# Kernel optimization log

Hardware: AMD Instinct MI355X
Metric: run time of the kernel (lower is better)

## Reference

```python
import jax, jax.numpy as jnp
import numpy as np

NUM_EXPERTS = 8
TOP_K = 2


def setup_inputs() -> dict:
    key = jax.random.key(0)
    ks = jax.random.split(key, 6)
    B, S, D, H, E = 4, 1024, 1024, 2048, NUM_EXPERTS
    x = jax.random.normal(ks[0], (B, S, D), dtype=jnp.float32)
    Wg = jax.random.normal(ks[1], (D, E), dtype=jnp.float32) * 0.02
    W1 = jax.random.normal(ks[2], (E, D, H), dtype=jnp.float32) * 0.02
    b1 = jax.random.normal(ks[3], (E, H), dtype=jnp.float32) * 0.02
    W2 = jax.random.normal(ks[4], (E, H, D), dtype=jnp.float32) * 0.02
    b2 = jax.random.normal(ks[5], (E, D), dtype=jnp.float32) * 0.02
    return {"x": x, "Wg": Wg, "W1": W1, "b1": b1, "W2": W2, "b2": b2}


def reference(x, Wg, W1, b1, W2, b2):
    B, S, D = x.shape
    E, _, H = W1.shape
    OUT = W2.shape[2]
    xm = x.reshape(-1, D)                      # [N, D], N = B*S
    # --- top-k gating (ProbabilitySamplerTopk): softmax over experts, take top-k ---
    logits = xm @ Wg                           # [N, E]
    probs = jax.nn.softmax(logits, axis=-1)
    topk_p, topk_i = jax.lax.top_k(probs, TOP_K)   # [N, K]
    # --- sort dispatched (token, expert) pairs by expert id (stable) ---
    flat_e = topk_i.reshape(-1)                # [N*K]
    flat_p = topk_p.reshape(-1)                # [N*K]
    order = jnp.argsort(flat_e)                # stable sort -> grouped by expert
    tok_idx = order // TOP_K                   # source token index (trunc-div by topK)
    e_sorted = flat_e[order]                   # [N*K]
    p_sorted = flat_p[order]                   # [N*K]
    xs = xm[tok_idx]                           # [N*K, D] expert-sorted inputs
    # --- grouped-GEMM experts: masked per-expert dense GEMM (E is small & fixed) ---
    y = jnp.zeros((xs.shape[0], OUT), dtype=xs.dtype)
    for e in range(E):
        h = jax.nn.relu(xs @ W1[e] + b1[e])    # [N*K, H]
        ye = h @ W2[e] + b2[e]                 # [N*K, OUT]
        m = (e_sorted == e)[:, None].astype(xs.dtype)
        y = y + m * ye
    # --- combine: multiply by gates, scatter-add back to token slots ---
    y = y * p_sorted[:, None]
    out = jnp.zeros((B * S, OUT), dtype=y.dtype).at[tok_idx].add(y)
    return out.reshape(B, S, OUT)
```

## Files before the change

### kernel.cpp

```cpp
#include <hip/hip_runtime.h>
#include <hip/hip_bf16.h>
#include <stdint.h>

typedef __bf16 bf16;
typedef __bf16 bf16x8 __attribute__((ext_vector_type(8)));
typedef __bf16 bf16x4 __attribute__((ext_vector_type(4)));
typedef float f32x4 __attribute__((ext_vector_type(4)));

#define N_TOK 4096
#define DDIM 1024
#define HDIM 2048
#define NPAIR 8192

__device__ __forceinline__ void gload16(const void* g, void* l) {
  __builtin_amdgcn_global_load_lds(
      (const __attribute__((address_space(1))) unsigned int*)g,
      (__attribute__((address_space(3))) unsigned int*)l, 16, 0, 0);
}

__global__ void transpose_cvt_kernel(const float* __restrict__ in, bf16* __restrict__ out,
                                     int R, int C) {
  __shared__ float tile[32][33];
  const float* ip = in + (size_t)blockIdx.z * R * C;
  bf16* op = out + (size_t)blockIdx.z * R * C;
  int r0 = blockIdx.y * 32, c0 = blockIdx.x * 32;
  int tr = threadIdx.x >> 3;
  int tc = (threadIdx.x & 7) * 4;
  float4 v = *(const float4*)(ip + (size_t)(r0 + tr) * C + c0 + tc);
  tile[tr][tc] = v.x; tile[tr][tc + 1] = v.y; tile[tr][tc + 2] = v.z; tile[tr][tc + 3] = v.w;
  __syncthreads();
  bf16x4 o = {(bf16)tile[tc + 0][tr], (bf16)tile[tc + 1][tr],
              (bf16)tile[tc + 2][tr], (bf16)tile[tc + 3][tr]};
  *(bf16x4*)(op + (size_t)(c0 + tr) * R + r0 + tc) = o;
}

__global__ void gate_kernel(const float* __restrict__ x, const float* __restrict__ Wg,
                            int2* __restrict__ ge, float2* __restrict__ gp,
                            bf16* __restrict__ xb, float* __restrict__ outp) {
  int t0 = blockIdx.x * 4;
  {
    float4 z = make_float4(0.f, 0.f, 0.f, 0.f);
    float4* ob = (float4*)(outp + (size_t)t0 * DDIM);
#pragma unroll
    for (int r = 0; r < 4; r++) ob[r * 256 + threadIdx.x] = z;
  }
  int t = t0 + (threadIdx.x >> 6);
  int lane = threadIdx.x & 63;
  const float* xr = x + (size_t)t * DDIM;
  bf16* xbr = xb + (size_t)t * DDIM;
  float a[8];
#pragma unroll
  for (int e = 0; e < 8; e++) a[e] = 0.f;
#pragma unroll
  for (int it = 0; it < 4; it++) {
    int d0 = it * 256 + lane * 4;
    float4 xv = *(const float4*)(xr + d0);
    bf16x4 o = {(bf16)xv.x, (bf16)xv.y, (bf16)xv.z, (bf16)xv.w};
    *(bf16x4*)(xbr + d0) = o;
    float xs[4] = {xv.x, xv.y, xv.z, xv.w};
#pragma unroll
    for (int dd = 0; dd < 4; dd++) {
      float4 w0 = *(const float4*)(Wg + (size_t)(d0 + dd) * 8);
      float4 w1 = *(const float4*)(Wg + (size_t)(d0 + dd) * 8 + 4);
      a[0] += xs[dd] * w0.x; a[1] += xs[dd] * w0.y; a[2] += xs[dd] * w0.z; a[3] += xs[dd] * w0.w;
      a[4] += xs[dd] * w1.x; a[5] += xs[dd] * w1.y; a[6] += xs[dd] * w1.z; a[7] += xs[dd] * w1.w;
    }
  }
#pragma unroll
  for (int off = 32; off >= 1; off >>= 1) {
#pragma unroll
    for (int e = 0; e < 8; e++) a[e] += __shfl_xor(a[e], off);
  }
  if (lane == 0) {
    float m = a[0];
#pragma unroll
    for (int e = 1; e < 8; e++) m = fmaxf(m, a[e]);
    float p[8]; float s = 0.f;
#pragma unroll
    for (int e = 0; e < 8; e++) { p[e] = expf(a[e] - m); s += p[e]; }
    float inv = 1.f / s;
    int i0 = 0; float v0 = a[0];
#pragma unroll
    for (int e = 1; e < 8; e++) if (a[e] > v0) { v0 = a[e]; i0 = e; }
    int i1 = -1; float v1 = -1e30f;
#pragma unroll
    for (int e = 0; e < 8; e++) if (e != i0 && a[e] > v1) { v1 = a[e]; i1 = e; }
    ge[t] = make_int2(i0, i1);
    gp[t] = make_float2(p[i0] * inv, p[i1] * inv);
  }
}

__global__ void sort_kernel(const int2* __restrict__ ge, const float2* __restrict__ gp,
                            int* __restrict__ tok, float* __restrict__ ps,
                            int* __restrict__ meta) {
  __shared__ int hist[8], runn[8], wc[16][8], wb[16][8], baseS[9];
  int tid = threadIdx.x;
  int lane = tid & 63, wv = tid >> 6;
  if (tid < 8) hist[tid] = 0;
  __syncthreads();
  for (int i = tid; i < NPAIR; i += 1024) {
    int2 g = ge[i >> 1];
    int e = (i & 1) ? g.y : g.x;
    atomicAdd(&hist[e], 1);
  }
  __syncthreads();
  if (tid == 0) {
    int b = 0, ts1 = 0;
    for (int e = 0; e < 8; e++) {
      baseS[e] = b; meta[e] = b;
      meta[9 + e] = ts1;  ts1 += (hist[e] + 127) / 128;
      b += hist[e];
    }
    baseS[8] = b; meta[8] = b; meta[17] = ts1;
  }
  __syncthreads();
  if (tid < 8) runn[tid] = baseS[tid];
  __syncthreads();
  for (int c = 0; c < 8; c++) {
    int i = c * 1024 + tid;
    int2 g = ge[i >> 1];
    int e = (i & 1) ? g.y : g.x;
    int rank = 0;
#pragma unroll
    for (int ee = 0; ee < 8; ee++) {
      unsigned long long b = __ballot(e == ee);
      if (e == ee) rank = __popcll(b & ((1ull << lane) - 1ull));
      if (lane == 0) wc[wv][ee] = __popcll(b);
    }
    __syncthreads();
    if (tid < 8) {
      int s = runn[tid];
      for (int w = 0; w < 16; w++) { wb[w][tid] = s; s += wc[w][tid]; }
      runn[tid] = s;
    }
    __syncthreads();
    int pos = wb[wv][e] + rank;
    tok[pos] = i >> 1;
    float2 p2 = gp[i >> 1];
    ps[pos] = (i & 1) ? p2.y : p2.x;
    __syncthreads();
  }
}

template <int KDIM, int NPE, bool FIRST, int NT>
__global__ __launch_bounds__(256, 2)
void moe_gemm_kernel(const bf16* __restrict__ A, const bf16* __restrict__ Bt,
                     const float* __restrict__ bias, const int* __restrict__ tok,
                     const float* __restrict__ ps, const int* __restrict__ meta,
                     bf16* __restrict__ hout, float* __restrict__ outp) {
  __shared__ bf16 lds[3][12288];
  constexpr int nk = KDIM / 32;

  int MTa = meta[17];
  int xcd = blockIdx.x & 7;
  int idx = blockIdx.x >> 3;
  int mLo = (MTa * xcd) >> 3;
  int mHi = (MTa * (xcd + 1)) >> 3;
  int cnt = mHi - mLo;
  if (idx >= cnt * NT) return;
  int tileN = idx / cnt;
  int tileM = mLo + idx - tileN * cnt;

  int e = 0;
#pragma unroll
  for (int k = 1; k < 8; k++) if (tileM >= meta[9 + k]) e = k;
  int row0 = meta[e] + (tileM - meta[9 + e]) * 128;
  int segEnd = meta[e + 1];
  int n0 = tileN * 256;

  int t = threadIdx.x;
  int swz = ((t & 3) ^ ((t >> 3) & 3)) * 8;
  const bf16* aSrc[2];
  const bf16* bSrc[4];
#pragma unroll
  for (int u = 0; u < 2; u++) {
    int row = u * 64 + (t >> 2);
    int gRow = row0 + row; if (gRow > NPAIR - 1) gRow = NPAIR - 1;
    int arow = FIRST ? tok[gRow] : gRow;
    aSrc[u] = A + (size_t)arow * KDIM + swz;
  }
#pragma unroll
  for (int u = 0; u < 4; u++) {
    int row = u * 64 + (t >> 2);
    bSrc[u] = Bt + ((size_t)e * NPE + n0 + row) * KDIM + swz;
  }

  int lane = t & 63, wv = t >> 6;
  int wm = wv >> 1, wn = wv & 1;
  int l15 = lane & 15, l4 = lane >> 4;
  int aOff[4], bOff[8];
#pragma unroll
  for (int m = 0; m < 4; m++) {
    int row = wm * 64 + m * 16 + l15;
    aOff[m] = row * 32 + ((l4 ^ ((row >> 1) & 3)) * 8);
  }
#pragma unroll
  for (int n = 0; n < 8; n++) {
    int row = wn * 128 + n * 16 + l15;
    bOff[n] = 4096 + row * 32 + ((l4 ^ ((row >> 1) & 3)) * 8);
  }

  f32x4 acc[4][8];
#pragma unroll
  for (int m = 0; m < 4; m++)
#pragma unroll
    for (int n = 0; n < 8; n++)
#pragma unroll
      for (int j = 0; j < 4; j++) acc[m][n][j] = 0.f;

  auto SA = [&](int j, int u) {
    gload16(aSrc[u] + j * 32, &lds[j % 3][0] + u * 2048 + t * 8);
  };
  auto SB = [&](int j, int u) {
    gload16(bSrc[u] + j * 32, &lds[j % 3][0] + 4096 + u * 2048 + t * 8);
  };

  SA(0, 0); SA(0, 1); SB(0, 0); SB(0, 1); SB(0, 2); SB(0, 3);
  SA(1, 0); SA(1, 1); SB(1, 0); SB(1, 1); SB(1, 2); SB(1, 3);
  asm volatile("s_waitcnt vmcnt(6)\n\ts_barrier" ::: "memory");

  for (int j = 0; j < nk; j++) {
    const bf16* sb = &lds[j % 3][0];
    bf16x8 af[4], bfr[4];
#pragma unroll
    for (int m = 0; m < 4; m++) af[m] = *(const bf16x8*)(sb + aOff[m]);
#pragma unroll
    for (int n = 0; n < 4; n++) bfr[n] = *(const bf16x8*)(sb + bOff[n]);
    if (j + 2 < nk) {
      SA(j + 2, 0); SA(j + 2, 1); SB(j + 2, 0);
      asm volatile("s_waitcnt vmcnt(3)\n\ts_barrier" ::: "memory");
    } else {
      asm volatile("s_waitcnt vmcnt(0)\n\ts_barrier" ::: "memory");
    }
    asm volatile("s_waitcnt lgkmcnt(0)" ::: "memory");
    __builtin_amdgcn_sched_barrier(0);
    __builtin_amdgcn_s_setprio(1);
#pragma unroll
    for (int m = 0; m < 4; m++)
#pragma unroll
      for (int n = 0; n < 4; n++)
        acc[m][n] = __builtin_amdgcn_mfma_f32_16x16x32_bf16(af[m], bfr[n], acc[m][n], 0, 0, 0);
    __builtin_amdgcn_s_setprio(0);
    __builtin_amdgcn_s_barrier();
#pragma unroll
    for (int n = 0; n < 4; n++) bfr[n] = *(const bf16x8*)(sb + bOff[4 + n]);
    if (j + 2 < nk) { SB(j + 2, 1); SB(j + 2, 2); SB(j + 2, 3); }
    __builtin_amdgcn_s_barrier();
    asm volatile("s_waitcnt lgkmcnt(0)" ::: "memory");
    __builtin_amdgcn_sched_barrier(0);
    __builtin_amdgcn_s_setprio(1);
#pragma unroll
    for (int m = 0; m < 4; m++)
#pragma unroll
      for (int n = 0; n < 4; n++)
        acc[m][4 + n] = __builtin_amdgcn_mfma_f32_16x16x32_bf16(af[m], bfr[n], acc[m][4 + n], 0, 0, 0);
    __builtin_amdgcn_s_setprio(0);
    __builtin_amdgcn_s_barrier();
  }

  int colb = n0 + wn * 128 + l15;
  float bia[8];
#pragma unroll
  for (int n = 0; n < 8; n++) bia[n] = bias[(size_t)e * NPE + colb + n * 16];
#pragma unroll
  for (int m = 0; m < 4; m++) {
#pragma unroll
    for (int jj = 0; jj < 4; jj++) {
      int gRow = row0 + wm * 64 + m * 16 + l4 * 4 + jj;
      if (gRow < segEnd) {
        if (FIRST) {
#pragma unroll
          for (int n = 0; n < 8; n++) {
            float v = acc[m][n][jj] + bia[n];
            v = fmaxf(v, 0.f);
            hout[(size_t)gRow * NPE + colb + n * 16] = (bf16)v;
          }
        } else {
          float pscale = ps[gRow];
          float* orow = outp + (size_t)tok[gRow] * DDIM;
#pragma unroll
          for (int n = 0; n < 8; n++) {
            float v = (acc[m][n][jj] + bia[n]) * pscale;
            atomicAdd(orow + colb + n * 16, v);
          }
        }
      }
    }
  }
}

extern "C" void kernel_launch(void* const* d_in, const int* in_sizes, int n_in,
                              void* d_out, int out_size, void* d_ws, size_t ws_size,
                              hipStream_t stream) {
  (void)in_sizes; (void)n_in; (void)out_size; (void)ws_size;
  const float* x  = (const float*)d_in[0];
  const float* Wg = (const float*)d_in[1];
  const float* W1 = (const float*)d_in[2];
  const float* b1 = (const float*)d_in[3];
  const float* W2 = (const float*)d_in[4];
  const float* b2 = (const float*)d_in[5];
  float* out = (float*)d_out;

  char* ws = (char*)d_ws;
  bf16*  xb   = (bf16*)(ws);
  bf16*  W1T  = (bf16*)(ws + (8ull  << 20));
  bf16*  W2T  = (bf16*)(ws + (40ull << 20));
  bf16*  hbuf = (bf16*)(ws + (72ull << 20));
  char*  ext  = ws + (104ull << 20);
  int2*   ge      = (int2*)(ext);
  float2* gp      = (float2*)(ext + (64u  << 10));
  int*    tok     = (int*)(ext + (128u << 10));
  float*  psarr   = (float*)(ext + (160u << 10));
  int*    meta    = (int*)(ext + (224u << 10));

  transpose_cvt_kernel<<<dim3(64, 32, 8), 256, 0, stream>>>(W1, W1T, 1024, 2048);
  transpose_cvt_kernel<<<dim3(32, 64, 8), 256, 0, stream>>>(W2, W2T, 2048, 1024);
  gate_kernel<<<1024, 256, 0, stream>>>(x, Wg, ge, gp, xb, out);
  sort_kernel<<<1, 1024, 0, stream>>>(ge, gp, tok, psarr, meta);
  moe_gemm_kernel<1024, 2048, true, 8><<<dim3(576), 256, 0, stream>>>(
      xb, W1T, b1, tok, psarr, meta, hbuf, nullptr);
  moe_gemm_kernel<2048, 1024, false, 4><<<dim3(288), 256, 0, stream>>>(
      hbuf, W2T, b2, tok, psarr, meta, nullptr, out);
}
```

Measured before the change: 203.1 us.

## Use 256x256 tiles with 512 threads and split-K for second GEMM

Both expert GEMMs move from 128x256 tiles with 256 threads to 256x256 tiles with 512 threads (8 waves), doubling per-block data reuse and reorganising the LDS pipeline. The second GEMM is split along K into two halves written to separate fp32 buffers, which a new combine kernel sums into the output. This is meant to raise arithmetic intensity and balance the grid to a fixed 320 blocks, at the cost of an extra zeroing pass, extra buffer traffic, more tile padding for small expert segments, and lower occupancy.

```diff
diff --git a/kernel.cpp b/kernel.cpp
--- a/kernel.cpp
+++ b/kernel.cpp
@@ -7,7 +7,6 @@
 typedef __bf16 bf16x4 __attribute__((ext_vector_type(4)));
 typedef float f32x4 __attribute__((ext_vector_type(4)));
 
-#define N_TOK 4096
 #define DDIM 1024
 #define HDIM 2048
 #define NPAIR 8192
@@ -36,13 +35,18 @@
 
 __global__ void gate_kernel(const float* __restrict__ x, const float* __restrict__ Wg,
                             int2* __restrict__ ge, float2* __restrict__ gp,
-                            bf16* __restrict__ xb, float* __restrict__ outp) {
+                            bf16* __restrict__ xb, float* __restrict__ y2a,
+                            float* __restrict__ y2b) {
   int t0 = blockIdx.x * 4;
   {
     float4 z = make_float4(0.f, 0.f, 0.f, 0.f);
-    float4* ob = (float4*)(outp + (size_t)t0 * DDIM);
-#pragma unroll
-    for (int r = 0; r < 4; r++) ob[r * 256 + threadIdx.x] = z;
+    float4* za = (float4*)(y2a + (size_t)t0 * DDIM);
+    float4* zb = (float4*)(y2b + (size_t)t0 * DDIM);
+#pragma unroll
+    for (int r = 0; r < 4; r++) {
+      za[r * 256 + threadIdx.x] = z;
+      zb[r * 256 + threadIdx.x] = z;
+    }
   }
   int t = t0 + (threadIdx.x >> 6);
   int lane = threadIdx.x & 63;
@@ -105,13 +109,13 @@
   }
   __syncthreads();
   if (tid == 0) {
-    int b = 0, ts1 = 0;
+    int b = 0, ts = 0;
     for (int e = 0; e < 8; e++) {
       baseS[e] = b; meta[e] = b;
-      meta[9 + e] = ts1;  ts1 += (hist[e] + 127) / 128;
+      meta[9 + e] = ts; ts += (hist[e] + 255) / 256;
       b += hist[e];
     }
-    baseS[8] = b; meta[8] = b; meta[17] = ts1;
+    baseS[8] = b; meta[8] = b; meta[17] = ts;
   }
   __syncthreads();
   if (tid < 8) runn[tid] = baseS[tid];
@@ -142,14 +146,19 @@
   }
 }
 
-template <int KDIM, int NPE, bool FIRST, int NT>
-__global__ __launch_bounds__(256, 2)
+template <bool FIRST>
+__global__ __launch_bounds__(512, 1)
 void moe_gemm_kernel(const bf16* __restrict__ A, const bf16* __restrict__ Bt,
                      const float* __restrict__ bias, const int* __restrict__ tok,
                      const float* __restrict__ ps, const int* __restrict__ meta,
-                     bf16* __restrict__ hout, float* __restrict__ outp) {
-  __shared__ bf16 lds[3][12288];
-  constexpr int nk = KDIM / 32;
+                     bf16* __restrict__ hout, float* __restrict__ y2a,
+                     float* __restrict__ y2b) {
+  constexpr int AK  = FIRST ? DDIM : HDIM;
+  constexpr int BK  = FIRST ? DDIM : HDIM;
+  constexpr int NPE = FIRST ? HDIM : DDIM;
+  constexpr int NT  = 8;
+  constexpr int nk  = 32;
+  __shared__ bf16 lds[3][16384];
 
   int MTa = meta[17];
   int xcd = blockIdx.x & 7;
@@ -164,129 +173,129 @@
   int e = 0;
 #pragma unroll
   for (int k = 1; k < 8; k++) if (tileM >= meta[9 + k]) e = k;
-  int row0 = meta[e] + (tileM - meta[9 + e]) * 128;
+  int row0 = meta[e] + (tileM - meta[9 + e]) * 256;
   int segEnd = meta[e + 1];
-  int n0 = tileN * 256;
+  int n0, kOff;
+  if (FIRST) { n0 = tileN * 256; kOff = 0; }
+  else       { n0 = (tileN & 3) * 256; kOff = (tileN >> 2) * 1024; }
 
   int t = threadIdx.x;
   int swz = ((t & 3) ^ ((t >> 3) & 3)) * 8;
   const bf16* aSrc[2];
-  const bf16* bSrc[4];
+  const bf16* bSrc[2];
 #pragma unroll
   for (int u = 0; u < 2; u++) {
-    int row = u * 64 + (t >> 2);
+    int row = u * 128 + (t >> 2);
     int gRow = row0 + row; if (gRow > NPAIR - 1) gRow = NPAIR - 1;
     int arow = FIRST ? tok[gRow] : gRow;
-    aSrc[u] = A + (size_t)arow * KDIM + swz;
-  }
-#pragma unroll
-  for (int u = 0; u < 4; u++) {
-    int row = u * 64 + (t >> 2);
-    bSrc[u] = Bt + ((size_t)e * NPE + n0 + row) * KDIM + swz;
+    aSrc[u] = A + (size_t)arow * AK + kOff + swz;
+    bSrc[u] = Bt + ((size_t)e * NPE + n0 + row) * BK + kOff + swz;
   }
 
   int lane = t & 63, wv = t >> 6;
-  int wm = wv >> 1, wn = wv & 1;
+  int wm = wv >> 2, wn = wv & 3;
   int l15 = lane & 15, l4 = lane >> 4;
-  int aOff[4], bOff[8];
-#pragma unroll
-  for (int m = 0; m < 4; m++) {
-    int row = wm * 64 + m * 16 + l15;
-    aOff[m] = row * 32 + ((l4 ^ ((row >> 1) & 3)) * 8);
-  }
-#pragma unroll
-  for (int n = 0; n < 8; n++) {
-    int row = wn * 128 + n * 16 + l15;
-    bOff[n] = 4096 + row * 32 + ((l4 ^ ((row >> 1) & 3)) * 8);
-  }
-
-  f32x4 acc[4][8];
-#pragma unroll
-  for (int m = 0; m < 4; m++)
-#pragma unroll
-    for (int n = 0; n < 8; n++)
-#pragma unroll
-      for (int j = 0; j < 4; j++) acc[m][n][j] = 0.f;
+  int aOff[8], bOff[4];
+#pragma unroll
+  for (int mf = 0; mf < 8; mf++) {
+    int row = wm * 128 + mf * 16 + l15;
+    aOff[mf] = row * 32 + ((l4 ^ ((row >> 1) & 3)) * 8);
+  }
+#pragma unroll
+  for (int nf = 0; nf < 4; nf++) {
+    int row = wn * 64 + nf * 16 + l15;
+    bOff[nf] = 8192 + row * 32 + ((l4 ^ ((row >> 1) & 3)) * 8);
+  }
+
+  f32x4 acc[8][4];
+#pragma unroll
+  for (int mf = 0; mf < 8; mf++)
+#pragma unroll
+    for (int nf = 0; nf < 4; nf++)
+#pragma unroll
+      for (int j = 0; j < 4; j++) acc[mf][nf][j] = 0.f;
 
   auto SA = [&](int j, int u) {
-    gload16(aSrc[u] + j * 32, &lds[j % 3][0] + u * 2048 + t * 8);
+    gload16(aSrc[u] + j * 32, &lds[j % 3][0] + u * 4096 + t * 8);
   };
   auto SB = [&](int j, int u) {
-    gload16(bSrc[u] + j * 32, &lds[j % 3][0] + 4096 + u * 2048 + t * 8);
+    gload16(bSrc[u] + j * 32, &lds[j % 3][0] + 8192 + u * 4096 + t * 8);
   };
 
-  SA(0, 0); SA(0, 1); SB(0, 0); SB(0, 1); SB(0, 2); SB(0, 3);
-  SA(1, 0); SA(1, 1); SB(1, 0); SB(1, 1); SB(1, 2); SB(1, 3);
-  asm volatile("s_waitcnt vmcnt(6)\n\ts_barrier" ::: "memory");
+  SA(0, 0); SA(0, 1); SB(0, 0); SB(0, 1);
+  SA(1, 0); SA(1, 1); SB(1, 0); SB(1, 1);
 
   for (int j = 0; j < nk; j++) {
     const bf16* sb = &lds[j % 3][0];
+    if (j + 2 < nk) { SA(j + 2, 0); SA(j + 2, 1); }
+    if (j + 2 < nk)      asm volatile("s_waitcnt vmcnt(6)\n\ts_barrier" ::: "memory");
+    else if (j + 1 < nk) asm volatile("s_waitcnt vmcnt(4)\n\ts_barrier" ::: "memory");
+    else                 asm volatile("s_waitcnt vmcnt(0)\n\ts_barrier" ::: "memory");
     bf16x8 af[4], bfr[4];
 #pragma unroll
-    for (int m = 0; m < 4; m++) af[m] = *(const bf16x8*)(sb + aOff[m]);
-#pragma unroll
-    for (int n = 0; n < 4; n++) bfr[n] = *(const bf16x8*)(sb + bOff[n]);
-    if (j + 2 < nk) {
-      SA(j + 2, 0); SA(j + 2, 1); SB(j + 2, 0);
-      asm volatile("s_waitcnt vmcnt(3)\n\ts_barrier" ::: "memory");
-    } else {
-      asm volatile("s_waitcnt vmcnt(0)\n\ts_barrier" ::: "memory");
-    }
+    for (int mf = 0; mf < 4; mf++) af[mf] = *(const bf16x8*)(sb + aOff[mf]);
+#pragma unroll
+    for (int nf = 0; nf < 4; nf++) bfr[nf] = *(const bf16x8*)(sb + bOff[nf]);
     asm volatile("s_waitcnt lgkmcnt(0)" ::: "memory");
     __builtin_amdgcn_sched_barrier(0);
     __builtin_amdgcn_s_setprio(1);
 #pragma unroll
-    for (int m = 0; m < 4; m++)
-#pragma unroll
-      for (int n = 0; n < 4; n++)
-        acc[m][n] = __builtin_amdgcn_mfma_f32_16x16x32_bf16(af[m], bfr[n], acc[m][n], 0, 0, 0);
+    for (int mf = 0; mf < 4; mf++)
+#pragma unroll
+      for (int nf = 0; nf < 4; nf++)
+        acc[mf][nf] = __builtin_amdgcn_mfma_f32_16x16x32_bf16(af[mf], bfr[nf], acc[mf][nf], 0, 0, 0);
     __builtin_amdgcn_s_setprio(0);
-    __builtin_amdgcn_s_barrier();
-#pragma unroll
-    for (int n = 0; n < 4; n++) bfr[n] = *(const bf16x8*)(sb + bOff[4 + n]);
-    if (j + 2 < nk) { SB(j + 2, 1); SB(j + 2, 2); SB(j + 2, 3); }
-    __builtin_amdgcn_s_barrier();
+    if (j + 2 < nk) { SB(j + 2, 0); SB(j + 2, 1); }
+#pragma unroll
+    for (int mf = 0; mf < 4; mf++) af[mf] = *(const bf16x8*)(sb + aOff[4 + mf]);
     asm volatile("s_waitcnt lgkmcnt(0)" ::: "memory");
     __builtin_amdgcn_sched_barrier(0);
     __builtin_amdgcn_s_setprio(1);
 #pragma unroll
-    for (int m = 0; m < 4; m++)
-#pragma unroll
-      for (int n = 0; n < 4; n++)
-        acc[m][4 + n] = __builtin_amdgcn_mfma_f32_16x16x32_bf16(af[m], bfr[n], acc[m][4 + n], 0, 0, 0);
+    for (int mf = 0; mf < 4; mf++)
+#pragma unroll
+      for (int nf = 0; nf < 4; nf++)
+        acc[4 + mf][nf] = __builtin_amdgcn_mfma_f32_16x16x32_bf16(af[mf], bfr[nf], acc[4 + mf][nf], 0, 0, 0);
     __builtin_amdgcn_s_setprio(0);
     __builtin_amdgcn_s_barrier();
   }
 
-  int colb = n0 + wn * 128 + l15;
-  float bia[8];
-#pragma unroll
-  for (int n = 0; n < 8; n++) bia[n] = bias[(size_t)e * NPE + colb + n * 16];
-#pragma unroll
-  for (int m = 0; m < 4; m++) {
+  int colb = n0 + wn * 64 + l15;
+  float bia[4];
+#pragma unroll
+  for (int nf = 0; nf < 4; nf++)
+    bia[nf] = (FIRST || kOff == 0) ? bias[(size_t)e * NPE + colb + nf * 16] : 0.f;
+  float* ybuf = FIRST ? nullptr : ((kOff == 0) ? y2a : y2b);
+#pragma unroll
+  for (int mf = 0; mf < 8; mf++) {
 #pragma unroll
     for (int jj = 0; jj < 4; jj++) {
-      int gRow = row0 + wm * 64 + m * 16 + l4 * 4 + jj;
+      int gRow = row0 + wm * 128 + mf * 16 + l4 * 4 + jj;
       if (gRow < segEnd) {
         if (FIRST) {
 #pragma unroll
-          for (int n = 0; n < 8; n++) {
-            float v = acc[m][n][jj] + bia[n];
-            v = fmaxf(v, 0.f);
-            hout[(size_t)gRow * NPE + colb + n * 16] = (bf16)v;
+          for (int nf = 0; nf < 4; nf++) {
+            float v = acc[mf][nf][jj] + bia[nf];
+            hout[(size_t)gRow * HDIM + colb + nf * 16] = (bf16)fmaxf(v, 0.f);
           }
         } else {
           float pscale = ps[gRow];
-          float* orow = outp + (size_t)tok[gRow] * DDIM;
-#pragma unroll
-          for (int n = 0; n < 8; n++) {
-            float v = (acc[m][n][jj] + bia[n]) * pscale;
-            atomicAdd(orow + colb + n * 16, v);
-          }
+          float* orow = ybuf + (size_t)tok[gRow] * DDIM;
+#pragma unroll
+          for (int nf = 0; nf < 4; nf++)
+            atomicAdd(orow + colb + nf * 16, (acc[mf][nf][jj] + bia[nf]) * pscale);
         }
       }
     }
   }
+}
+
+__global__ void combine_kernel(const float* __restrict__ a, const float* __restrict__ b,
+                               float* __restrict__ out) {
+  int i = blockIdx.x * 256 + threadIdx.x;
+  f32x4 va = ((const f32x4*)a)[i];
+  f32x4 vb = ((const f32x4*)b)[i];
+  ((f32x4*)out)[i] = va + vb;
 }
 
 extern "C" void kernel_launch(void* const* d_in, const int* in_sizes, int n_in,
@@ -306,7 +315,9 @@
   bf16*  W1T  = (bf16*)(ws + (8ull  << 20));
   bf16*  W2T  = (bf16*)(ws + (40ull << 20));
   bf16*  hbuf = (bf16*)(ws + (72ull << 20));
-  char*  ext  = ws + (104ull << 20);
+  float* y2a  = (float*)(ws + (104ull << 20));
+  float* y2b  = (float*)(ws + (120ull << 20));
+  char*  ext  = ws + (136ull << 20);
   int2*   ge      = (int2*)(ext);
   float2* gp      = (float2*)(ext + (64u  << 10));
   int*    tok     = (int*)(ext + (128u << 10));
@@ -315,10 +326,11 @@
 
   transpose_cvt_kernel<<<dim3(64, 32, 8), 256, 0, stream>>>(W1, W1T, 1024, 2048);
   transpose_cvt_kernel<<<dim3(32, 64, 8), 256, 0, stream>>>(W2, W2T, 2048, 1024);
-  gate_kernel<<<1024, 256, 0, stream>>>(x, Wg, ge, gp, xb, out);
+  gate_kernel<<<1024, 256, 0, stream>>>(x, Wg, ge, gp, xb, y2a, y2b);
   sort_kernel<<<1, 1024, 0, stream>>>(ge, gp, tok, psarr, meta);
-  moe_gemm_kernel<1024, 2048, true, 8><<<dim3(576), 256, 0, stream>>>(
-      xb, W1T, b1, tok, psarr, meta, hbuf, nullptr);
-  moe_gemm_kernel<2048, 1024, false, 4><<<dim3(288), 256, 0, stream>>>(
-      hbuf, W2T, b2, tok, psarr, meta, nullptr, out);
-}
+  moe_gemm_kernel<true><<<dim3(320), 512, 0, stream>>>(
+      xb, W1T, b1, tok, psarr, meta, hbuf, nullptr, nullptr);
+  moe_gemm_kernel<false><<<dim3(320), 512, 0, stream>>>(
+      hbuf, W2T, b2, tok, psarr, meta, nullptr, y2a, y2b);
+  combine_kernel<<<4096, 256, 0, stream>>>(y2a, y2b, out);
+}
```

Result: slower. 265.3 us (+30.6%).
